# Performance work log

Measured on AMD Instinct MI355X. Metric: run time of the kernel, lower is better.

The kernel has to match this reference:

```python
import jax, jax.numpy as jnp
import numpy as np
import math

NUM_HEADS = 16
HEAD_DIM = 64
D_MODEL = NUM_HEADS * HEAD_DIM  # 1024
B, S = 4, 2048

def setup_inputs() -> dict:
    key = jax.random.key(0)
    ks = jax.random.split(key, 8)
    sd = 1.0 / math.sqrt(D_MODEL)
    return {
        "hidden_states": jax.random.normal(ks[0], (B, S, D_MODEL), jnp.float32),
        "attention_mask": jnp.zeros((B, 1, 1, S), jnp.float32),
        "Wq": jax.random.normal(ks[1], (D_MODEL, D_MODEL), jnp.float32) * sd,
        "bq": jnp.zeros((D_MODEL,), jnp.float32),
        "Wk": jax.random.normal(ks[2], (D_MODEL, D_MODEL), jnp.float32) * sd,
        "bk": jnp.zeros((D_MODEL,), jnp.float32),
        "Wv": jax.random.normal(ks[3], (D_MODEL, D_MODEL), jnp.float32) * sd,
        "bv": jnp.zeros((D_MODEL,), jnp.float32),
    }

def _split_heads(x):
    # [B, S, D] -> [B, H, S, hd]
    b, s, _ = x.shape
    return x.reshape(b, s, NUM_HEADS, HEAD_DIM).transpose(0, 2, 1, 3)

def reference(hidden_states, attention_mask, Wq, bq, Wk, bk, Wv, bv):
    # Linear projections (torch nn.Linear: x @ W.T + b)
    q = _split_heads(hidden_states @ Wq.T + bq)
    k = _split_heads(hidden_states @ Wk.T + bk)
    v = _split_heads(hidden_states @ Wv.T + bv)
    scale = 1.0 / math.sqrt(HEAD_DIM)
    # [B, H, Sq, Sk] attention scores, fully materialized as in the original
    scores = jnp.einsum("bhqd,bhkd->bhqk", q, k) * scale + attention_mask
    # relusq replacement for softmax
    probs = jnp.square(jax.nn.relu(scores))
    ctx = jnp.einsum("bhqk,bhkd->bhqd", probs, v)  # [B, H, S, hd]
    b = ctx.shape[0]
    return ctx.transpose(0, 2, 1, 3).reshape(b, -1, D_MODEL)
```

## Files before the change

kernel.cpp:

```cpp
#include <hip/hip_runtime.h>


typedef __bf16 bf16x8 __attribute__((ext_vector_type(8)));
typedef __bf16 bf16x4 __attribute__((ext_vector_type(4)));
typedef short  s16x4  __attribute__((ext_vector_type(4)));
typedef float  f32x4  __attribute__((ext_vector_type(4)));
typedef float  floatx4 __attribute__((ext_vector_type(4)));

#define MFMA16(a, b, c) __builtin_amdgcn_mfma_f32_16x16x32_bf16(a, b, c, 0, 0, 0)
#define MFMA16K16(a, b, c) \
    __builtin_amdgcn_mfma_f32_16x16x16bf16_1k(a, b, c, 0, 0, 0)

#define WAITCNT_VM4() __builtin_amdgcn_s_waitcnt(0x0F74)

__device__ __forceinline__ void glds16(const __bf16* g, __bf16* l) {
    __builtin_amdgcn_global_load_lds(
        (const __attribute__((address_space(1))) void*)g,
        (__attribute__((address_space(3))) void*)l, 16, 0, 0);
}

__global__ __launch_bounds__(256) void convert_kernel(
    const float* __restrict__ X, const float* __restrict__ Wq,
    const float* __restrict__ Wk, const float* __restrict__ Wv,
    __bf16* __restrict__ Xb, __bf16* __restrict__ Wqb,
    __bf16* __restrict__ Wkb, __bf16* __restrict__ Wvb)
{
    int blk = blockIdx.x;
    const float* src; __bf16* dst; size_t base;
    if (blk < 4096)      { src = X;  dst = Xb;  base = (size_t)blk * 2048; }
    else if (blk < 4608) { src = Wq; dst = Wqb; base = (size_t)(blk - 4096) * 2048; }
    else if (blk < 5120) { src = Wk; dst = Wkb; base = (size_t)(blk - 4608) * 2048; }
    else                 { src = Wv; dst = Wvb; base = (size_t)(blk - 5120) * 2048; }
    size_t off = base + (size_t)threadIdx.x * 8;
    floatx4 a = *(const floatx4*)(src + off);
    floatx4 c = *(const floatx4*)(src + off + 4);
    bf16x8 o;
    o[0] = (__bf16)a[0]; o[1] = (__bf16)a[1]; o[2] = (__bf16)a[2]; o[3] = (__bf16)a[3];
    o[4] = (__bf16)c[0]; o[5] = (__bf16)c[1]; o[6] = (__bf16)c[2]; o[7] = (__bf16)c[3];
    *(bf16x8*)(dst + off) = o;
}

__global__ __launch_bounds__(256) void qkv_gemm_kernel(
    const __bf16* __restrict__ Xb,
    const __bf16* __restrict__ Wqb, const __bf16* __restrict__ Wkb,
    const __bf16* __restrict__ Wvb,
    const float* __restrict__ bq, const float* __restrict__ bk,
    const float* __restrict__ bv,
    __bf16* __restrict__ qws, __bf16* __restrict__ kws, __bf16* __restrict__ vws)
{
    __shared__ __bf16 As[128 * 64];
    __shared__ __bf16 Bs[128 * 64];

    const int tid  = threadIdx.x;
    const int lane = tid & 63;
    const int wave = tid >> 6;
    const int wm   = (wave >> 1) * 64;
    const int wn   = (wave & 1) * 64;
    const int quad = lane >> 4;
    const int l16  = lane & 15;
    const int m0   = blockIdx.y * 128;

    const int sel = blockIdx.x >> 3;
    const bool vmode = (sel == 2);
    const __bf16* Wb = (sel == 0) ? Wqb : (sel == 1) ? Wkb : Wvb;
    const float* bias = (sel == 0) ? bq : (sel == 1) ? bk : bv;
    __bf16* outp = (sel == 0) ? qws : (sel == 1) ? kws : vws;
    const int n0 = (blockIdx.x & 7) * 128;

    const __bf16* Pa = vmode ? As : Bs;
    const __bf16* Pb = vmode ? Bs : As;
    const int woffA = vmode ? wm : wn;
    const int woffB = vmode ? wn : wm;

    f32x4 acc[4][4] = {};

    for (int k0 = 0; k0 < 1024; k0 += 64) {
        __syncthreads();
        #pragma unroll
        for (int i = 0; i < 4; ++i) {
            int r = wave * 32 + i * 8 + (lane >> 3);
            int c = (lane & 7) ^ (r & 7);
            glds16(Xb + (size_t)(m0 + r) * 1024 + k0 + c * 8,
                   &As[(wave * 32 + i * 8) * 64]);
            glds16(Wb + (size_t)(n0 + r) * 1024 + k0 + c * 8,
                   &Bs[(wave * 32 + i * 8) * 64]);
        }
        __syncthreads();

        #pragma unroll
        for (int kk8 = 0; kk8 < 8; kk8 += 4) {
            bf16x8 af[4], bfr[4];
            #pragma unroll
            for (int a = 0; a < 4; ++a)
                af[a] = *(const bf16x8*)&Pa[(woffA + a * 16 + l16) * 64 +
                                            (((kk8 + quad) ^ (l16 & 7)) * 8)];
            #pragma unroll
            for (int bb = 0; bb < 4; ++bb)
                bfr[bb] = *(const bf16x8*)&Pb[(woffB + bb * 16 + l16) * 64 +
                                              (((kk8 + quad) ^ (l16 & 7)) * 8)];
            #pragma unroll
            for (int a = 0; a < 4; ++a)
                #pragma unroll
                for (int bb = 0; bb < 4; ++bb)
                    acc[a][bb] = MFMA16(af[a], bfr[bb], acc[a][bb]);
        }
    }

    if (!vmode) {
        #pragma unroll
        for (int a = 0; a < 4; ++a) {
            int n = n0 + woffA + a * 16 + quad * 4;
            floatx4 bv4 = *(const floatx4*)&bias[n];
            int h = n >> 6, d0 = n & 63;
            #pragma unroll
            for (int bb = 0; bb < 4; ++bb) {
                int m = m0 + woffB + bb * 16 + l16;
                int bt = m >> 11, s = m & 2047;
                bf16x4 o;
                #pragma unroll
                for (int r = 0; r < 4; ++r)
                    o[r] = (__bf16)(acc[a][bb][r] + bv4[r]);
                *(bf16x4*)&outp[((size_t)(bt * 16 + h) * 2048 + s) * 64 + d0] = o;
            }
        }
    } else {
        #pragma unroll
        for (int a = 0; a < 4; ++a) {
            int m = m0 + woffA + a * 16 + quad * 4;
            int bt = m >> 11, s0 = m & 2047;
            #pragma unroll
            for (int bb = 0; bb < 4; ++bb) {
                int n = n0 + woffB + bb * 16 + l16;
                float bvv = bias[n];
                int h = n >> 6, d = n & 63;
                bf16x4 o;
                #pragma unroll
                for (int r = 0; r < 4; ++r)
                    o[r] = (__bf16)(acc[a][bb][r] + bvv);
                *(bf16x4*)&outp[((size_t)(bt * 16 + h) * 64 + d) * 2048 + s0] = o;
            }
        }
    }
}

__global__ __launch_bounds__(256, 2) void attn_kernel(
    const __bf16* __restrict__ Q, const __bf16* __restrict__ K,
    const __bf16* __restrict__ Vt, const float* __restrict__ mask,
    float* __restrict__ out)
{
    __shared__ __bf16 Ks[2][64 * 64];
    __shared__ __bf16 Vs[2][64 * 64];

    const int tid  = threadIdx.x;
    const int lane = tid & 63;
    const int wave = tid >> 6;
    const int quad = lane >> 4;
    const int l16  = lane & 15;
    const int bh   = blockIdx.y;
    const int b    = bh >> 4;
    const int h    = bh & 15;
    const int q0   = blockIdx.x * 256 + wave * 64;

    const __bf16* Qb = Q  + (size_t)bh * 2048 * 64;
    const __bf16* Kb = K  + (size_t)bh * 2048 * 64;
    const __bf16* Vb = Vt + (size_t)bh * 64 * 2048;
    const float*  mb = mask + b * 2048;

    const int srow = (lane >> 3);
    const int schk = (lane & 7);

    bf16x8 aq[4][2];
    #pragma unroll
    for (int qi = 0; qi < 4; ++qi)
        #pragma unroll
        for (int kcd = 0; kcd < 2; ++kcd)
            aq[qi][kcd] = *(const bf16x8*)(Qb +
                (size_t)(q0 + qi * 16 + l16) * 64 + kcd * 32 + quad * 8);

    f32x4 co[4][4] = {};

    #pragma unroll
    for (int i = 0; i < 2; ++i) {
        int rb = wave * 16 + i * 8;
        int r  = rb + srow;
        int c  = schk ^ (r & 7);
        glds16(Kb + (size_t)r * 64 + c * 8, &Ks[0][rb * 64]);
        glds16(Vb + (size_t)r * 2048 + 0 + c * 8, &Vs[0][rb * 64]);
    }

    for (int t = 0; t < 32; ++t) {
        const int k0 = t * 64;
        const int kn = (k0 + 64) & 2047;
        const int nb = (t + 1) & 1;
        #pragma unroll
        for (int i = 0; i < 2; ++i) {
            int rb = wave * 16 + i * 8;
            int r  = rb + srow;
            int c  = schk ^ (r & 7);
            glds16(Kb + (size_t)(kn + r) * 64 + c * 8, &Ks[nb][rb * 64]);
            glds16(Vb + (size_t)r * 2048 + kn + c * 8, &Vs[nb][rb * 64]);
        }
        WAITCNT_VM4();
        __syncthreads();

        const __bf16* Kt = &Ks[t & 1][0];
        const __bf16* Vtile = &Vs[t & 1][0];

        bf16x4 pf[4][4];
        #pragma unroll
        for (int ki = 0; ki < 4; ++ki) {
            f32x4 st[4] = {};
            #pragma unroll
            for (int kcd = 0; kcd < 2; ++kcd) {
                int key = ki * 16 + l16;
                bf16x8 ak = *(const bf16x8*)&Kt[key * 64 +
                    (((kcd * 4 + quad) ^ (key & 7)) * 8)];
                #pragma unroll
                for (int qi = 0; qi < 4; ++qi)
                    st[qi] = MFMA16(ak, aq[qi][kcd], st[qi]);
            }
            floatx4 mk = *(const floatx4*)&mb[k0 + ki * 16 + quad * 4];
            #pragma unroll
            for (int qi = 0; qi < 4; ++qi) {
                bf16x4 pv;
                #pragma unroll
                for (int r = 0; r < 4; ++r) {
                    float x = st[qi][r] * 0.125f + mk[r];
                    x = fmaxf(x, 0.0f);
                    pv[r] = (__bf16)(x * x);
                }
                pf[ki][qi] = pv;
            }
        }

        #pragma unroll
        for (int ki = 0; ki < 4; ++ki) {
            bf16x4 vb[4];
            #pragma unroll
            for (int dt = 0; dt < 4; ++dt) {
                int d = dt * 16 + l16;
                int g = ki * 2 + (quad >> 1);
                vb[dt] = *(const bf16x4*)&Vtile[d * 64 +
                    ((g ^ (d & 7)) * 8) + (quad & 1) * 4];
            }
            #pragma unroll
            for (int qi = 0; qi < 4; ++qi) {
                s16x4 pa = __builtin_bit_cast(s16x4, pf[ki][qi]);
                #pragma unroll
                for (int dt = 0; dt < 4; ++dt)
                    co[qi][dt] = MFMA16K16(pa,
                        __builtin_bit_cast(s16x4, vb[dt]), co[qi][dt]);
            }
        }
        __syncthreads();
    }

    #pragma unroll
    for (int qi = 0; qi < 4; ++qi)
        #pragma unroll
        for (int r = 0; r < 4; ++r) {
            int q = q0 + qi * 16 + quad * 4 + r;
            float* orow = &out[(((size_t)b * 2048 + q) * 16 + h) * 64];
            #pragma unroll
            for (int dt = 0; dt < 4; ++dt)
                orow[dt * 16 + l16] = co[qi][dt][r];
        }
}

extern "C" void kernel_launch(void* const* d_in, const int* in_sizes, int n_in,
                              void* d_out, int out_size, void* d_ws, size_t ws_size,
                              hipStream_t stream) {
    const float* hidden = (const float*)d_in[0];
    const float* mask   = (const float*)d_in[1];
    const float* Wq     = (const float*)d_in[2];
    const float* bq     = (const float*)d_in[3];
    const float* Wk     = (const float*)d_in[4];
    const float* bk     = (const float*)d_in[5];
    const float* Wv     = (const float*)d_in[6];
    const float* bv     = (const float*)d_in[7];
    float* out = (float*)d_out;

    __bf16* qws = (__bf16*)d_ws;
    __bf16* kws = qws + (size_t)64 * 2048 * 64;
    __bf16* vws = kws + (size_t)64 * 2048 * 64;
    __bf16* Xb  = vws + (size_t)64 * 2048 * 64;
    __bf16* Wqb = Xb  + (size_t)8192 * 1024;
    __bf16* Wkb = Wqb + (size_t)1024 * 1024;
    __bf16* Wvb = Wkb + (size_t)1024 * 1024;

    dim3 blk(256);
    convert_kernel<<<dim3(5632), blk, 0, stream>>>(hidden, Wq, Wk, Wv,
                                                   Xb, Wqb, Wkb, Wvb);
    qkv_gemm_kernel<<<dim3(24, 64), blk, 0, stream>>>(Xb, Wqb, Wkb, Wvb,
                                                      bq, bk, bv, qws, kws, vws);
    attn_kernel<<<dim3(8, 64), blk, 0, stream>>>(qws, kws, vws, mask, out);
}
```

Before: 272.0 us.

## Split attention block into 8 waves of 32 queries each for higher occupancy

The attention kernel now launches 512 threads per block, with each of 8 waves handling 32 query rows instead of 4 waves handling 64. This halves the per-wave Q and accumulator register arrays and raises launch bounds to allow more waves per CU, to better hide latency. Each thread now issues a single K and V async load per tile, the wait count is adjusted to match, and __syncthreads is replaced with a raw s_barrier. The trade-off is less register reuse of each K/V LDS read, since every wave reads the same LDS data but does fewer MFMAs per read.

Measured after the change: 272.3 us. Within noise of the previous version (+0.1%).

```diff
diff --git a/kernel.cpp b/kernel.cpp
--- a/kernel.cpp
+++ b/kernel.cpp
@@ -11,7 +11,8 @@
 #define MFMA16K16(a, b, c) \
     __builtin_amdgcn_mfma_f32_16x16x16bf16_1k(a, b, c, 0, 0, 0)
 
-#define WAITCNT_VM4() __builtin_amdgcn_s_waitcnt(0x0F74)
+#define WAITCNT_VM2() __builtin_amdgcn_s_waitcnt(0x0F72)
+#define BARRIER() __builtin_amdgcn_s_barrier()
 
 __device__ __forceinline__ void glds16(const __bf16* g, __bf16* l) {
     __builtin_amdgcn_global_load_lds(
@@ -143,7 +144,7 @@
     }
 }
 
-__global__ __launch_bounds__(256, 2) void attn_kernel(
+__global__ __launch_bounds__(512, 4) void attn_kernel(
     const __bf16* __restrict__ Q, const __bf16* __restrict__ K,
     const __bf16* __restrict__ Vt, const float* __restrict__ mask,
     float* __restrict__ out)
@@ -159,69 +160,58 @@
     const int bh   = blockIdx.y;
     const int b    = bh >> 4;
     const int h    = bh & 15;
-    const int q0   = blockIdx.x * 256 + wave * 64;
+    const int q0   = blockIdx.x * 256 + wave * 32;
 
     const __bf16* Qb = Q  + (size_t)bh * 2048 * 64;
     const __bf16* Kb = K  + (size_t)bh * 2048 * 64;
     const __bf16* Vb = Vt + (size_t)bh * 64 * 2048;
     const float*  mb = mask + b * 2048;
 
-    const int srow = (lane >> 3);
-    const int schk = (lane & 7);
-
-    bf16x8 aq[4][2];
+    const int rb = wave * 8;
+    const int sr = rb + (lane >> 3);
+    const int sc = ((lane & 7) ^ (sr & 7)) * 8;
+
+    bf16x8 aq[2][2];
     #pragma unroll
-    for (int qi = 0; qi < 4; ++qi)
+    for (int qi = 0; qi < 2; ++qi)
         #pragma unroll
         for (int kcd = 0; kcd < 2; ++kcd)
             aq[qi][kcd] = *(const bf16x8*)(Qb +
                 (size_t)(q0 + qi * 16 + l16) * 64 + kcd * 32 + quad * 8);
 
-    f32x4 co[4][4] = {};
-
-    #pragma unroll
-    for (int i = 0; i < 2; ++i) {
-        int rb = wave * 16 + i * 8;
-        int r  = rb + srow;
-        int c  = schk ^ (r & 7);
-        glds16(Kb + (size_t)r * 64 + c * 8, &Ks[0][rb * 64]);
-        glds16(Vb + (size_t)r * 2048 + 0 + c * 8, &Vs[0][rb * 64]);
-    }
+    f32x4 co[2][4] = {};
+
+    glds16(Kb + (size_t)sr * 64 + sc, &Ks[0][rb * 64]);
+    glds16(Vb + (size_t)sr * 2048 + sc, &Vs[0][rb * 64]);
 
     for (int t = 0; t < 32; ++t) {
         const int k0 = t * 64;
         const int kn = (k0 + 64) & 2047;
         const int nb = (t + 1) & 1;
-        #pragma unroll
-        for (int i = 0; i < 2; ++i) {
-            int rb = wave * 16 + i * 8;
-            int r  = rb + srow;
-            int c  = schk ^ (r & 7);
-            glds16(Kb + (size_t)(kn + r) * 64 + c * 8, &Ks[nb][rb * 64]);
-            glds16(Vb + (size_t)r * 2048 + kn + c * 8, &Vs[nb][rb * 64]);
-        }
-        WAITCNT_VM4();
-        __syncthreads();
+        glds16(Kb + (size_t)(kn + sr) * 64 + sc, &Ks[nb][rb * 64]);
+        glds16(Vb + (size_t)sr * 2048 + kn + sc, &Vs[nb][rb * 64]);
+        WAITCNT_VM2();
+        BARRIER();
 
         const __bf16* Kt = &Ks[t & 1][0];
         const __bf16* Vtile = &Vs[t & 1][0];
 
-        bf16x4 pf[4][4];
+        bf16x4 pf[4][2];
         #pragma unroll
         for (int ki = 0; ki < 4; ++ki) {
-            f32x4 st[4] = {};
+            f32x4 st[2] = {};
             #pragma unroll
             for (int kcd = 0; kcd < 2; ++kcd) {
                 int key = ki * 16 + l16;
                 bf16x8 ak = *(const bf16x8*)&Kt[key * 64 +
                     (((kcd * 4 + quad) ^ (key & 7)) * 8)];
                 #pragma unroll
-                for (int qi = 0; qi < 4; ++qi)
+                for (int qi = 0; qi < 2; ++qi)
                     st[qi] = MFMA16(ak, aq[qi][kcd], st[qi]);
             }
             floatx4 mk = *(const floatx4*)&mb[k0 + ki * 16 + quad * 4];
             #pragma unroll
-            for (int qi = 0; qi < 4; ++qi) {
+            for (int qi = 0; qi < 2; ++qi) {
                 bf16x4 pv;
                 #pragma unroll
                 for (int r = 0; r < 4; ++r) {
@@ -235,28 +225,28 @@
 
         #pragma unroll
         for (int ki = 0; ki < 4; ++ki) {
-            bf16x4 vb[4];
+            bf16x4 vb4[4];
             #pragma unroll
             for (int dt = 0; dt < 4; ++dt) {
                 int d = dt * 16 + l16;
                 int g = ki * 2 + (quad >> 1);
-                vb[dt] = *(const bf16x4*)&Vtile[d * 64 +
+                vb4[dt] = *(const bf16x4*)&Vtile[d * 64 +
                     ((g ^ (d & 7)) * 8) + (quad & 1) * 4];
             }
             #pragma unroll
-            for (int qi = 0; qi < 4; ++qi) {
+            for (int qi = 0; qi < 2; ++qi) {
                 s16x4 pa = __builtin_bit_cast(s16x4, pf[ki][qi]);
                 #pragma unroll
                 for (int dt = 0; dt < 4; ++dt)
                     co[qi][dt] = MFMA16K16(pa,
-                        __builtin_bit_cast(s16x4, vb[dt]), co[qi][dt]);
-            }
-        }
-        __syncthreads();
+                        __builtin_bit_cast(s16x4, vb4[dt]), co[qi][dt]);
+            }
+        }
+        BARRIER();
     }
 
     #pragma unroll
-    for (int qi = 0; qi < 4; ++qi)
+    for (int qi = 0; qi < 2; ++qi)
         #pragma unroll
         for (int r = 0; r < 4; ++r) {
             int q = q0 + qi * 16 + quad * 4 + r;
@@ -288,10 +278,10 @@
     __bf16* Wkb = Wqb + (size_t)1024 * 1024;
     __bf16* Wvb = Wkb + (size_t)1024 * 1024;
 
-    dim3 blk(256);
-    convert_kernel<<<dim3(5632), blk, 0, stream>>>(hidden, Wq, Wk, Wv,
-                                                   Xb, Wqb, Wkb, Wvb);
-    qkv_gemm_kernel<<<dim3(24, 64), blk, 0, stream>>>(Xb, Wqb, Wkb, Wvb,
-                                                      bq, bk, bv, qws, kws, vws);
-    attn_kernel<<<dim3(8, 64), blk, 0, stream>>>(qws, kws, vws, mask, out);
-}
+    convert_kernel<<<dim3(5632), dim3(256), 0, stream>>>(hidden, Wq, Wk, Wv,
+                                                         Xb, Wqb, Wkb, Wvb);
+    qkv_gemm_kernel<<<dim3(24, 64), dim3(256), 0, stream>>>(Xb, Wqb, Wkb, Wvb,
+                                                            bq, bk, bv,
+                                                            qws, kws, vws);
+    attn_kernel<<<dim3(8, 64), dim3(512), 0, stream>>>(qws, kws, vws, mask, out);
+}
```
